# Kernel tuning notes

Hardware: AMD Instinct MI355X
Metric: run time of the kernel (lower is better)

The kernel has to match this reference:

```python
import jax, jax.numpy as jnp
import numpy as np

B, H, D_OUT, T_STEPS = 256, 1024, 128, 128


def setup_inputs() -> dict:
    key = jax.random.key(0)
    ks = jax.random.split(key, 7)
    s = 1.0 / np.sqrt(H)
    return {
        "x": jax.random.normal(ks[0], (B, H), dtype=jnp.float32),
        "W_ih": jax.random.normal(ks[1], (4 * H, H), dtype=jnp.float32) * s,
        "W_hh": jax.random.normal(ks[2], (4 * H, H), dtype=jnp.float32) * s,
        "b_ih": jax.random.normal(ks[3], (4 * H,), dtype=jnp.float32) * s,
        "b_hh": jax.random.normal(ks[4], (4 * H,), dtype=jnp.float32) * s,
        "W_out": jax.random.normal(ks[5], (D_OUT, H), dtype=jnp.float32) * s,
        "b_out": jax.random.normal(ks[6], (D_OUT,), dtype=jnp.float32) * s,
        "T": T_STEPS,
    }


def reference(x, W_ih, W_hh, b_ih, b_hh, W_out, b_out, T):
    # first input is x. h0 = c0 = 0. PyTorch gate order: i, f, g, o.
    Hd = x.shape[1]
    b = b_ih + b_hh  # [4H]

    def step(carry, _):
        inp, h, c = carry  # each [B, H]
        gates = inp @ W_ih.T + h @ W_hh.T + b  # [B, 4H]
        i_g, f_g, g_g, o_g = jnp.split(gates, 4, axis=-1)
        c_new = jax.nn.sigmoid(f_g) * c + jax.nn.sigmoid(i_g) * jnp.tanh(g_g)
        h_new = jax.nn.sigmoid(o_g) * jnp.tanh(c_new)
        return (h_new, h_new, c_new), h_new

    zeros = jnp.zeros_like(x)
    _, seq = jax.lax.scan(step, (x, zeros, zeros), None, length=T)  # [T, B, H]
    out = seq @ W_out.T + b_out            # [T, B, D_out] (dropout is identity at eval)
    return jnp.transpose(out, (1, 0, 2))   # [B, T, D_out]
```

## Files before the change

### kernel.cpp

```cpp
#include <hip/hip_runtime.h>

typedef _Float16 half8 __attribute__((ext_vector_type(8)));
typedef _Float16 half4 __attribute__((ext_vector_type(4)));
typedef float    f32x4 __attribute__((ext_vector_type(4)));
typedef unsigned long long u64x2 __attribute__((ext_vector_type(2)));

constexpr int Bt   = 256;
constexpr int Hd   = 1024;
constexpr int G4   = 4096;
constexpr int Ts   = 128;
constexpr int DOUT = 128;

constexpr int NGROUP   = 8;
constexpr int WG_PER_G = 32;
constexpr int NWG      = NGROUP * WG_PER_G;
constexpr int NTHR     = 512;
constexpr int GROWS    = Bt / NGROUP;

constexpr size_t SEQ_T = (size_t)32 * 256 * 64;

constexpr size_t OFF_WSUM = 0;
constexpr size_t OFF_WIH  = OFF_WSUM + (size_t)G4 * Hd * 2;
constexpr size_t OFF_WOUT = OFF_WIH  + (size_t)G4 * Hd * 2;
constexpr size_t OFF_X    = OFF_WOUT + (size_t)DOUT * Hd * 2;
constexpr size_t OFF_BSUM = OFF_X    + (size_t)Bt * Hd * 2;
constexpr size_t OFF_BAR  = OFF_BSUM + (size_t)G4 * 4;
constexpr size_t OFF_SEQ  = OFF_BAR  + 131072;
constexpr size_t WS_NEED  = OFF_SEQ  + (size_t)Ts * SEQ_T;

__device__ __forceinline__ float fast_sig(float x) {
    return 1.f / (1.f + __expf(-x));
}
__device__ __forceinline__ float fast_tanh(float x) {
    float ax = fabsf(x);
    float e  = __expf(-2.f * ax);
    float t  = (1.f - e) / (1.f + e);
    return copysignf(t, x);
}

__device__ __forceinline__ void gload_lds16(const void* g, void* l) {
    __builtin_amdgcn_global_load_lds(
        (const __attribute__((address_space(1))) void*)g,
        (__attribute__((address_space(3))) void*)l, 16, 0, 0);
}
__device__ __forceinline__ void store16_wt(void* gp, u64x2 v) {
    asm volatile("global_store_dwordx4 %0, %1, off sc0 sc1"
                 :: "v"(gp), "v"(v) : "memory");
}
__device__ __forceinline__ void store4_wt(unsigned* gp, unsigned v) {
    asm volatile("global_store_dword %0, %1, off sc0 sc1"
                 :: "v"(gp), "v"(v) : "memory");
}
__device__ __forceinline__ unsigned load4_cp(const unsigned* gp) {
    unsigned v;
    asm volatile("global_load_dword %0, %1, off sc0 sc1\n\t"
                 "s_waitcnt vmcnt(0)"
                 : "=v"(v) : "v"(gp) : "memory");
    return v;
}

__global__ void prep_kernel(const float* __restrict__ Wih, const float* __restrict__ Whh,
                            const float* __restrict__ bih, const float* __restrict__ bhh,
                            const float* __restrict__ x,   const float* __restrict__ Wout,
                            _Float16* __restrict__ wsum16, _Float16* __restrict__ wih16,
                            _Float16* __restrict__ wout16, _Float16* __restrict__ x16,
                            float* __restrict__ bsum, unsigned* __restrict__ bar) {
    const int i0     = blockIdx.x * blockDim.x + threadIdx.x;
    const int stride = gridDim.x * blockDim.x;

    for (int i = i0; i < G4 * Hd / 4; i += stride) {
        f32x4 a = ((const f32x4*)Wih)[i];
        f32x4 b = ((const f32x4*)Whh)[i];
        half4 hs, hi;
        #pragma unroll
        for (int j = 0; j < 4; ++j) {
            hs[j] = (_Float16)(a[j] + b[j]);
            hi[j] = (_Float16)a[j];
        }
        ((half4*)wsum16)[i] = hs;
        ((half4*)wih16)[i]  = hi;
    }
    for (int i = i0; i < DOUT * Hd / 4; i += stride) {
        f32x4 a = ((const f32x4*)Wout)[i];
        half4 h;
        #pragma unroll
        for (int j = 0; j < 4; ++j) h[j] = (_Float16)a[j];
        ((half4*)wout16)[i] = h;
    }
    for (int i = i0; i < Bt * Hd / 4; i += stride) {
        f32x4 a = ((const f32x4*)x)[i];
        half4 h;
        #pragma unroll
        for (int j = 0; j < 4; ++j) h[j] = (_Float16)a[j];
        const int row = i >> 8;
        const int e   = (i & 255) * 4;
        const int jb  = e >> 5;
        const int c   = e & 31;
        ((half4*)x16)[(jb * 256 + row) * 8 + (c >> 2)] = h;
    }
    for (int i = i0; i < G4; i += stride) bsum[i] = bih[i] + bhh[i];
    for (int i = i0; i < 32768; i += stride)
        __hip_atomic_store(bar + i, 0u, __ATOMIC_RELAXED, __HIP_MEMORY_SCOPE_AGENT);
}

__launch_bounds__(NTHR, 2)
__global__ void lstm_kernel(const _Float16* __restrict__ wsum16,
                            const _Float16* __restrict__ wih16,
                            const _Float16* __restrict__ wout16,
                            const _Float16* __restrict__ x16,
                            const float* __restrict__ bsum,
                            const float* __restrict__ bout,
                            _Float16* __restrict__ seq,
                            float* __restrict__ out,
                            unsigned* __restrict__ bar) {
    __shared__ char smem[65536];

    const int bid = blockIdx.x;
    const int g   = bid & 7;
    const int wgi = bid >> 3;
    const int tid = threadIdx.x;
    const int wv  = tid >> 6;
    const int l   = tid & 63;
    const int lr  = l & 15;
    const int lk  = l >> 4;
    const int ks  = wv & 3;
    const int jg  = wv >> 2;
    const int j0  = wgi * 32 + jg * 16;
    const int brow0 = g * GROWS;
    const bool lead = (ks == 0);

    unsigned* gflags = bar + (size_t)g * 4096;

    float bias[4];
    #pragma unroll
    for (int gg = 0; gg < 4; ++gg) bias[gg] = bsum[gg * Hd + j0 + lr];

    half8 Bf[4][8];
    auto loadB = [&](const _Float16* __restrict__ W) {
        #pragma unroll
        for (int gg = 0; gg < 4; ++gg)
            #pragma unroll
            for (int kk = 0; kk < 8; ++kk)
                Bf[gg][kk] = *(const half8*)(W + (size_t)(gg * Hd + j0 + lr) * Hd
                                               + ks * 256 + kk * 32 + lk * 8);
    };

    const char* x16c = (const char*)x16;
    char*       seqc = (char*)seq;

    auto stageS = [&](char* Abase, const char* srcb, int rbase) {
        #pragma unroll
        for (int s = 0; s < 4; ++s) {
            const int i   = wv * 4 + s;
            const int row = i >> 1;
            const int gb  = ((i & 1) * 64 + l) ^ (row & 7);
            const int jb  = gb >> 2;
            const int q   = gb & 3;
            gload_lds16(srcb + ((size_t)(jb * 256 + rbase + row)) * 64 + q * 16,
                        Abase + i * 1024);
        }
    };

    auto mfmaS = [&](char* Abase, f32x4* acc) {
        #pragma unroll
        for (int gg = 0; gg < 4; ++gg) acc[gg] = f32x4{0.f,0.f,0.f,0.f};
        #pragma unroll
        for (int kk = 0; kk < 8; ++kk) {
            const int bb = (ks * 32 + kk * 4 + lk) ^ (lr & 7);
            half8 a = *(const half8*)(Abase + lr * 2048 + bb * 16);
            #pragma unroll
            for (int gg = 0; gg < 4; ++gg)
                acc[gg] = __builtin_amdgcn_mfma_f32_16x16x32_f16(a, Bf[gg][kk], acc[gg], 0,0,0);
        }
    };

    auto dumpS = [&](char* Abase, const f32x4* acc) {
        char* dst = Abase + (size_t)(jg * 3 + (ks - 1)) * 4096;
        #pragma unroll
        for (int gg = 0; gg < 4; ++gg)
            *(f32x4*)(dst + gg * 1024 + l * 16) = acc[gg];
    };

    auto finishS = [&](char* Abase, f32x4* acc, f32x4& cc, int S, int t) {
        #pragma unroll
        for (int s = 0; s < 3; ++s) {
            const char* src = Abase + (size_t)(jg * 3 + s) * 4096;
            #pragma unroll
            for (int gg = 0; gg < 4; ++gg)
                acc[gg] += *(const f32x4*)(src + gg * 1024 + l * 16);
        }
        char* hst = Abase + 24576 + jg * 512;
        #pragma unroll
        for (int r = 0; r < 4; ++r) {
            float ig = fast_sig (acc[0][r] + bias[0]);
            float fg = fast_sig (acc[1][r] + bias[1]);
            float gv = fast_tanh(acc[2][r] + bias[2]);
            float og = fast_sig (acc[3][r] + bias[3]);
            float cn = fg * cc[r] + ig * gv;
            cc[r] = cn;
            float hv = og * fast_tanh(cn);
            *(_Float16*)(hst + (lk * 4 + r) * 32 + lr * 2) = (_Float16)hv;
        }
        if (l < 32) {
            const int row = l >> 1;
            const int q   = l & 1;
            u64x2 v = *(const u64x2*)(hst + row * 32 + q * 16);
            char* gp = seqc + (size_t)t * SEQ_T
                     + ((size_t)(wgi * 256 + brow0 + S * 16 + row)) * 64
                     + jg * 32 + q * 16;
            store16_wt(gp, v);
        }
        asm volatile("s_waitcnt vmcnt(0)" ::: "memory");
        if (l == 0)
            store4_wt(gflags + wgi * 128 + S * 64 + jg * 32, (unsigned)(t + 1));
    };

    auto pollS = [&](int S, unsigned tgt) {
        const unsigned* p = gflags + (l & 31) * 128 + S * 64 + (l >> 5) * 32;
        while (true) {
            unsigned v = load4_cp(p);
            if (__all(v >= tgt)) break;
            __builtin_amdgcn_s_sleep(1);
        }
    };

    char* A_P = smem;
    char* A_Q = smem + 32768;
    f32x4 cP = {0.f,0.f,0.f,0.f}, cQ = {0.f,0.f,0.f,0.f};
    f32x4 acc[4];

    loadB(wih16);

    stageS(A_P, x16c, brow0);
    __syncthreads();

    #pragma unroll 1
    for (int t = 0; t < Ts; ++t) {
        const char* srcQ = (t == 0) ? x16c : (seqc + (size_t)(t - 1) * SEQ_T);

        mfmaS(A_P, acc);
        __syncthreads();
        if (wv == 0) pollS(1, (unsigned)t);
        else if (!lead) dumpS(A_P, acc);
        __syncthreads();
        stageS(A_Q, srcQ, brow0 + 16);
        if (lead) finishS(A_P, acc, cP, 0, t);
        __syncthreads();

        mfmaS(A_Q, acc);
        __syncthreads();
        if (t < Ts - 1) {
            if (wv == 0) pollS(0, (unsigned)(t + 1));
            else if (!lead) dumpS(A_Q, acc);
            __syncthreads();
            stageS(A_P, seqc + (size_t)t * SEQ_T, brow0);
        } else {
            if (!lead) dumpS(A_Q, acc);
            __syncthreads();
        }
        if (lead) finishS(A_Q, acc, cQ, 1, t);
        if (t == 0) loadB(wsum16);
        __syncthreads();
    }

    if (wv == 0) {
        const unsigned* p0 = gflags + (l & 31) * 128 + (l >> 5) * 32;
        while (true) {
            unsigned a = load4_cp(p0);
            unsigned b = load4_cp(p0 + 64);
            if (__all((a >= (unsigned)Ts) & (b >= (unsigned)Ts))) break;
            __builtin_amdgcn_s_sleep(1);
        }
    }
    __syncthreads();

    {
        const int idx  = wgi * 8 + wv;
        const int t_   = idx >> 1;
        const int bb16 = brow0 + (idx & 1) * 16;
        const int row  = bb16 + lr;
        const char* ab = seqc + (size_t)t_ * SEQ_T + (size_t)row * 64 + lk * 16;

        f32x4 oacc[8];
        #pragma unroll
        for (int ni = 0; ni < 8; ++ni) oacc[ni] = f32x4{0.f,0.f,0.f,0.f};

        #pragma unroll 2
        for (int k0 = 0; k0 < Hd; k0 += 32) {
            half8 a = *(const half8*)(ab + (size_t)k0 * 512);
            #pragma unroll
            for (int ni = 0; ni < 8; ++ni) {
                half8 bf = *(const half8*)(wout16 + (size_t)(ni * 16 + lr) * Hd + lk * 8 + k0);
                oacc[ni] = __builtin_amdgcn_mfma_f32_16x16x32_f16(a, bf, oacc[ni], 0,0,0);
            }
        }
        #pragma unroll
        for (int ni = 0; ni < 8; ++ni) {
            const int d  = ni * 16 + lr;
            const float bo = bout[d];
            #pragma unroll
            for (int r = 0; r < 4; ++r) {
                const int b = bb16 + lk * 4 + r;
                out[(size_t)b * (Ts * DOUT) + t_ * DOUT + d] = oacc[ni][r] + bo;
            }
        }
    }
}

extern "C" void kernel_launch(void* const* d_in, const int* in_sizes, int n_in,
                              void* d_out, int out_size, void* d_ws, size_t ws_size,
                              hipStream_t stream) {
    const float* x    = (const float*)d_in[0];
    const float* Wih  = (const float*)d_in[1];
    const float* Whh  = (const float*)d_in[2];
    const float* bih  = (const float*)d_in[3];
    const float* bhh  = (const float*)d_in[4];
    const float* Wout = (const float*)d_in[5];
    const float* bout = (const float*)d_in[6];

    if (ws_size < WS_NEED) return;

    char* ws = (char*)d_ws;
    _Float16* wsum16 = (_Float16*)(ws + OFF_WSUM);
    _Float16* wih16  = (_Float16*)(ws + OFF_WIH);
    _Float16* wout16 = (_Float16*)(ws + OFF_WOUT);
    _Float16* x16    = (_Float16*)(ws + OFF_X);
    float*    bsum   = (float*)(ws + OFF_BSUM);
    unsigned* bar    = (unsigned*)(ws + OFF_BAR);
    _Float16* seq    = (_Float16*)(ws + OFF_SEQ);
    float*    outp   = (float*)d_out;

    hipLaunchKernelGGL(prep_kernel, dim3(1024), dim3(256), 0, stream,
                       Wih, Whh, bih, bhh, x, Wout,
                       wsum16, wih16, wout16, x16, bsum, bar);

    void* args[] = { &wsum16, &wih16, &wout16, &x16, &bsum,
                     (void*)&bout, &seq, &outp, &bar };
    hipLaunchCooperativeKernel((void*)lstm_kernel, dim3(NWG), dim3(NTHR),
                               args, 0, stream);
}
```

Before: 985.5 us.

## Split batch slices into four 8-row stages with atomic-counter flags

Splits each group's 32 batch rows into four 8-row sub-slices processed in a rotating four-buffer LDS pipeline instead of two 16-row halves. Replaces the per-workgroup flag arrays, which were polled with a wave-wide all-reduce, with per-(slice, timestep) counters bumped by atomic adds and polled on a single address. The aim is deeper overlap of the cross-workgroup dependency wait with MFMA work and cheaper synchronisation. In exchange, half of each 16-row MFMA tile is wasted on duplicated rows and there are twice as many barriers per step. Atomic contention on the shared counters is a further risk.

Measured after the change: 1.658 ms. +68.3%, slower.

```diff
diff --git a/kernel.cpp b/kernel.cpp
--- a/kernel.cpp
+++ b/kernel.cpp
@@ -15,7 +15,7 @@
 constexpr int WG_PER_G = 32;
 constexpr int NWG      = NGROUP * WG_PER_G;
 constexpr int NTHR     = 512;
-constexpr int GROWS    = Bt / NGROUP;
+constexpr int GROWS    = 32;
 
 constexpr size_t SEQ_T = (size_t)32 * 256 * 64;
 
@@ -25,7 +25,8 @@
 constexpr size_t OFF_X    = OFF_WOUT + (size_t)DOUT * Hd * 2;
 constexpr size_t OFF_BSUM = OFF_X    + (size_t)Bt * Hd * 2;
 constexpr size_t OFF_BAR  = OFF_BSUM + (size_t)G4 * 4;
-constexpr size_t OFF_SEQ  = OFF_BAR  + 131072;
+constexpr size_t BAR_SZ   = (size_t)NGROUP * 4 * Ts * 128;
+constexpr size_t OFF_SEQ  = OFF_BAR  + BAR_SZ;
 constexpr size_t WS_NEED  = OFF_SEQ  + (size_t)Ts * SEQ_T;
 
 __device__ __forceinline__ float fast_sig(float x) {
@@ -45,10 +46,6 @@
 }
 __device__ __forceinline__ void store16_wt(void* gp, u64x2 v) {
     asm volatile("global_store_dwordx4 %0, %1, off sc0 sc1"
-                 :: "v"(gp), "v"(v) : "memory");
-}
-__device__ __forceinline__ void store4_wt(unsigned* gp, unsigned v) {
-    asm volatile("global_store_dword %0, %1, off sc0 sc1"
                  :: "v"(gp), "v"(v) : "memory");
 }
 __device__ __forceinline__ unsigned load4_cp(const unsigned* gp) {
@@ -57,6 +54,10 @@
                  "s_waitcnt vmcnt(0)"
                  : "=v"(v) : "v"(gp) : "memory");
     return v;
+}
+__device__ __forceinline__ void atomic_add_nr(unsigned* gp, unsigned v) {
+    asm volatile("global_atomic_add %0, %1, off"
+                 :: "v"(gp), "v"(v) : "memory");
 }
 
 __global__ void prep_kernel(const float* __restrict__ Wih, const float* __restrict__ Whh,
@@ -99,7 +100,7 @@
         ((half4*)x16)[(jb * 256 + row) * 8 + (c >> 2)] = h;
     }
     for (int i = i0; i < G4; i += stride) bsum[i] = bih[i] + bhh[i];
-    for (int i = i0; i < 32768; i += stride)
+    for (int i = i0; i < (int)(BAR_SZ / 4); i += stride)
         __hip_atomic_store(bar + i, 0u, __ATOMIC_RELAXED, __HIP_MEMORY_SCOPE_AGENT);
 }
 
@@ -129,7 +130,9 @@
     const int brow0 = g * GROWS;
     const bool lead = (ks == 0);
 
-    unsigned* gflags = bar + (size_t)g * 4096;
+    auto cptr = [&](int S, int tt) -> unsigned* {
+        return bar + (((size_t)(g * 4 + S) * Ts + tt) << 5);
+    };
 
     float bias[4];
     #pragma unroll
@@ -150,8 +153,8 @@
 
     auto stageS = [&](char* Abase, const char* srcb, int rbase) {
         #pragma unroll
-        for (int s = 0; s < 4; ++s) {
-            const int i   = wv * 4 + s;
+        for (int s = 0; s < 2; ++s) {
+            const int i   = wv * 2 + s;
             const int row = i >> 1;
             const int gb  = ((i & 1) * 64 + l) ^ (row & 7);
             const int jb  = gb >> 2;
@@ -161,114 +164,106 @@
         }
     };
 
-    auto mfmaS = [&](char* Abase, f32x4* acc) {
-        #pragma unroll
-        for (int gg = 0; gg < 4; ++gg) acc[gg] = f32x4{0.f,0.f,0.f,0.f};
-        #pragma unroll
-        for (int kk = 0; kk < 8; ++kk) {
-            const int bb = (ks * 32 + kk * 4 + lk) ^ (lr & 7);
-            half8 a = *(const half8*)(Abase + lr * 2048 + bb * 16);
-            #pragma unroll
-            for (int gg = 0; gg < 4; ++gg)
-                acc[gg] = __builtin_amdgcn_mfma_f32_16x16x32_f16(a, Bf[gg][kk], acc[gg], 0,0,0);
-        }
-    };
-
-    auto dumpS = [&](char* Abase, const f32x4* acc) {
-        char* dst = Abase + (size_t)(jg * 3 + (ks - 1)) * 4096;
-        #pragma unroll
-        for (int gg = 0; gg < 4; ++gg)
-            *(f32x4*)(dst + gg * 1024 + l * 16) = acc[gg];
-    };
-
-    auto finishS = [&](char* Abase, f32x4* acc, f32x4& cc, int S, int t) {
-        #pragma unroll
-        for (int s = 0; s < 3; ++s) {
-            const char* src = Abase + (size_t)(jg * 3 + s) * 4096;
-            #pragma unroll
-            for (int gg = 0; gg < 4; ++gg)
-                acc[gg] += *(const f32x4*)(src + gg * 1024 + l * 16);
-        }
-        char* hst = Abase + 24576 + jg * 512;
-        #pragma unroll
-        for (int r = 0; r < 4; ++r) {
-            float ig = fast_sig (acc[0][r] + bias[0]);
-            float fg = fast_sig (acc[1][r] + bias[1]);
-            float gv = fast_tanh(acc[2][r] + bias[2]);
-            float og = fast_sig (acc[3][r] + bias[3]);
-            float cn = fg * cc[r] + ig * gv;
-            cc[r] = cn;
-            float hv = og * fast_tanh(cn);
-            *(_Float16*)(hst + (lk * 4 + r) * 32 + lr * 2) = (_Float16)hv;
-        }
-        if (l < 32) {
-            const int row = l >> 1;
-            const int q   = l & 1;
-            u64x2 v = *(const u64x2*)(hst + row * 32 + q * 16);
-            char* gp = seqc + (size_t)t * SEQ_T
-                     + ((size_t)(wgi * 256 + brow0 + S * 16 + row)) * 64
-                     + jg * 32 + q * 16;
-            store16_wt(gp, v);
-        }
+    f32x4 c[4];
+    #pragma unroll
+    for (int S = 0; S < 4; ++S) c[S] = f32x4{0.f,0.f,0.f,0.f};
+
+    loadB(wih16);
+    stageS(smem, x16c, brow0);
+    __syncthreads();
+
+    #pragma unroll 1
+    for (int t4 = 0; t4 < Ts; ++t4) {
+        #pragma unroll
+        for (int S = 0; S < 4; ++S) {
+            char* A    = smem + S * 16384;
+            char* Anx  = smem + ((S + 1) & 3) * 16384;
+            char* Admp = smem + ((S + 2) & 3) * 16384;
+            const int  p        = t4 * 4 + S;
+            const int  tp       = (S == 3) ? t4 + 1 : t4;
+            const bool do_stage = (p != Ts * 4 - 1);
+
+            f32x4 acc[4];
+            #pragma unroll
+            for (int gg = 0; gg < 4; ++gg) acc[gg] = f32x4{0.f,0.f,0.f,0.f};
+            #pragma unroll
+            for (int kk = 0; kk < 8; ++kk) {
+                const int bb = (ks * 32 + kk * 4 + lk) ^ (lr & 7);
+                half8 a = *(const half8*)(A + (lr & 7) * 2048 + bb * 16);
+                #pragma unroll
+                for (int gg = 0; gg < 4; ++gg)
+                    acc[gg] = __builtin_amdgcn_mfma_f32_16x16x32_f16(a, Bf[gg][kk], acc[gg], 0,0,0);
+            }
+            __syncthreads();
+
+            if (!lead) {
+                if (lk < 2) {
+                    char* dst = Admp + (jg * 3 + ks - 1) * 2048;
+                    #pragma unroll
+                    for (int gg = 0; gg < 4; ++gg)
+                        *(f32x4*)(dst + gg * 512 + lr * 32 + lk * 16) = acc[gg];
+                }
+                if (wv == 1 && do_stage && tp >= 1) {
+                    unsigned* cp = cptr((S + 1) & 3, tp - 1);
+                    while (load4_cp(cp) < 64u) __builtin_amdgcn_s_sleep(1);
+                }
+            }
+            __syncthreads();
+
+            if (lead && l == 0 && p > 0)
+                atomic_add_nr(cptr((S + 3) & 3, (S == 0) ? t4 - 1 : t4), 1u);
+
+            if (do_stage) {
+                const char* src = (tp == 0) ? x16c : (seqc + (size_t)(tp - 1) * SEQ_T);
+                stageS(Anx, src, brow0 + ((S + 1) & 3) * 8);
+            }
+
+            if (lead && lk < 2) {
+                #pragma unroll
+                for (int s = 0; s < 3; ++s) {
+                    const char* srcd = Admp + (jg * 3 + s) * 2048;
+                    #pragma unroll
+                    for (int gg = 0; gg < 4; ++gg)
+                        acc[gg] += *(const f32x4*)(srcd + gg * 512 + lr * 32 + lk * 16);
+                }
+                char* hst = Admp + 12288 + jg * 256;
+                #pragma unroll
+                for (int r = 0; r < 4; ++r) {
+                    float ig = fast_sig (acc[0][r] + bias[0]);
+                    float fg = fast_sig (acc[1][r] + bias[1]);
+                    float gv = fast_tanh(acc[2][r] + bias[2]);
+                    float og = fast_sig (acc[3][r] + bias[3]);
+                    float cn = fg * c[S][r] + ig * gv;
+                    c[S][r] = cn;
+                    float hv = og * fast_tanh(cn);
+                    *(_Float16*)(hst + (lk * 4 + r) * 32 + lr * 2) = (_Float16)hv;
+                }
+            }
+            if (lead) {
+                asm volatile("s_waitcnt lgkmcnt(0)" ::: "memory");
+                if (l < 16) {
+                    const char* hst = Admp + 12288 + jg * 256;
+                    u64x2 v = *(const u64x2*)(hst + (l >> 1) * 32 + (l & 1) * 16);
+                    char* gp = seqc + (size_t)t4 * SEQ_T
+                             + ((size_t)(wgi * 256 + brow0 + S * 8 + (l >> 1))) * 64
+                             + jg * 32 + (l & 1) * 16;
+                    store16_wt(gp, v);
+                }
+            }
+            if (t4 == 0 && S == 3) loadB(wsum16);
+            __syncthreads();
+        }
+    }
+
+    if (lead) {
         asm volatile("s_waitcnt vmcnt(0)" ::: "memory");
-        if (l == 0)
-            store4_wt(gflags + wgi * 128 + S * 64 + jg * 32, (unsigned)(t + 1));
-    };
-
-    auto pollS = [&](int S, unsigned tgt) {
-        const unsigned* p = gflags + (l & 31) * 128 + S * 64 + (l >> 5) * 32;
+        if (l == 0) atomic_add_nr(cptr(3, Ts - 1), 1u);
+    }
+    if (wv == 0) {
+        unsigned* cp = cptr(l & 3, Ts - 1);
         while (true) {
-            unsigned v = load4_cp(p);
-            if (__all(v >= tgt)) break;
-            __builtin_amdgcn_s_sleep(1);
-        }
-    };
-
-    char* A_P = smem;
-    char* A_Q = smem + 32768;
-    f32x4 cP = {0.f,0.f,0.f,0.f}, cQ = {0.f,0.f,0.f,0.f};
-    f32x4 acc[4];
-
-    loadB(wih16);
-
-    stageS(A_P, x16c, brow0);
-    __syncthreads();
-
-    #pragma unroll 1
-    for (int t = 0; t < Ts; ++t) {
-        const char* srcQ = (t == 0) ? x16c : (seqc + (size_t)(t - 1) * SEQ_T);
-
-        mfmaS(A_P, acc);
-        __syncthreads();
-        if (wv == 0) pollS(1, (unsigned)t);
-        else if (!lead) dumpS(A_P, acc);
-        __syncthreads();
-        stageS(A_Q, srcQ, brow0 + 16);
-        if (lead) finishS(A_P, acc, cP, 0, t);
-        __syncthreads();
-
-        mfmaS(A_Q, acc);
-        __syncthreads();
-        if (t < Ts - 1) {
-            if (wv == 0) pollS(0, (unsigned)(t + 1));
-            else if (!lead) dumpS(A_Q, acc);
-            __syncthreads();
-            stageS(A_P, seqc + (size_t)t * SEQ_T, brow0);
-        } else {
-            if (!lead) dumpS(A_Q, acc);
-            __syncthreads();
-        }
-        if (lead) finishS(A_Q, acc, cQ, 1, t);
-        if (t == 0) loadB(wsum16);
-        __syncthreads();
-    }
-
-    if (wv == 0) {
-        const unsigned* p0 = gflags + (l & 31) * 128 + (l >> 5) * 32;
-        while (true) {
-            unsigned a = load4_cp(p0);
-            unsigned b = load4_cp(p0 + 64);
-            if (__all((a >= (unsigned)Ts) & (b >= (unsigned)Ts))) break;
+            unsigned v = load4_cp(cp);
+            if (__all(v >= 64u)) break;
             __builtin_amdgcn_s_sleep(1);
         }
     }
```
